# Kernel optimization log

Measured on AMD Instinct MI355X. Metric: run time of the kernel, lower is better.

Reference implementation:

```python
import jax, jax.numpy as jnp
import numpy as np

B, S0, S1 = 4, 768, 256
T = S0 + S1
D0, D1 = 2048, 1024
N, K, H = 8, 1, 256  # num_heads, num_kv_heads, head_dim
G = N // K
BIG_NEG = -2.3819763e38


def _apply_rope(x, positions, max_wavelength=10000):
    # x: [B, L, Hn, Hd]; positions: [B, L] float32
    half = x.shape[-1] // 2
    freq_exponents = (2.0 / x.shape[-1]) * jnp.arange(half, dtype=jnp.float32)
    timescale = max_wavelength ** freq_exponents
    radians = positions[..., None] / timescale[None, None, :]   # [B, L, half]
    radians = radians[..., None, :]                             # [B, L, 1, half]
    sin, cos = jnp.sin(radians), jnp.cos(radians)
    x1, x2 = jnp.split(x, 2, axis=-1)
    res = jnp.concatenate([x1 * cos - x2 * sin, x2 * cos + x1 * sin], axis=-1)
    return res.astype(x.dtype)


def setup_inputs() -> dict:
    key = jax.random.key(0)
    ks = jax.random.split(key, 8)
    x0 = jax.random.normal(ks[0], (B, S0, D0), dtype=jnp.float32)
    x1 = jax.random.normal(ks[1], (B, S1, D1), dtype=jnp.float32)
    positions = jnp.broadcast_to(jnp.arange(T, dtype=jnp.float32), (B, T))
    # causal mask [B, 1, T, T]
    attn_mask = jnp.broadcast_to(jnp.tril(jnp.ones((T, T), dtype=bool)), (B, 1, T, T))
    # lecun_normal-style init: std = 1/sqrt(fan_in=width)
    q0_w = jax.random.normal(ks[2], (N, D0, H), dtype=jnp.float32) * (D0 ** -0.5)
    kv0_w = jax.random.normal(ks[3], (2, K, D0, H), dtype=jnp.float32) * (D0 ** -0.5)
    q1_w = jax.random.normal(ks[4], (N, D1, H), dtype=jnp.float32) * (D1 ** -0.5)
    kv1_w = jax.random.normal(ks[5], (2, K, D1, H), dtype=jnp.float32) * (D1 ** -0.5)
    o0_w = jax.random.normal(ks[6], (N, H, D0), dtype=jnp.float32) * ((N * H) ** -0.5)
    o1_w = jax.random.normal(ks[7], (N, H, D1), dtype=jnp.float32) * ((N * H) ** -0.5)
    return {"x0": x0, "x1": x1, "positions": positions, "attn_mask": attn_mask,
            "q0_w": q0_w, "kv0_w": kv0_w, "q1_w": q1_w, "kv1_w": kv1_w,
            "o0_w": o0_w, "o1_w": o1_w}


def reference(x0, x1, positions, attn_mask, q0_w, kv0_w, q1_w, kv1_w, o0_w, o1_w):
    dtype = x0.dtype
    # per-stream GQA projections (num_kv_heads != num_heads path)
    q_a = jnp.einsum('BTD,NDH->BTNH', x0, q0_w)
    kv_a = jnp.einsum('BSD,CKDH->CBSKH', x0, kv0_w)
    q_b = jnp.einsum('BTD,NDH->BTNH', x1, q1_w)
    kv_b = jnp.einsum('BSD,CKDH->CBSKH', x1, kv1_w)
    # concat streams along sequence
    q = jnp.concatenate([q_a, q_b], axis=1)                 # [B, T, N, H]
    k = jnp.concatenate([kv_a[0], kv_b[0]], axis=1)         # [B, T, K, H]
    v = jnp.concatenate([kv_a[1], kv_b[1]], axis=1)         # [B, T, K, H]
    # inline RoPE + query scaling
    q = _apply_rope(q, positions) * (H ** -0.5)
    k = _apply_rope(k, positions)
    # GQA grouping: N = K * G
    qg = q.reshape(q.shape[0], q.shape[1], K, G, H)          # [B, T, K, G, H]
    logits = jnp.einsum('BTKGH,BSKH->BKGTS', qg, k,
                        preferred_element_type=jnp.float32)  # fp32 scores
    masked = jnp.where(attn_mask[:, :, None, :, :], logits, BIG_NEG)
    probs = jax.nn.softmax(masked, axis=-1).astype(dtype)
    encoded = jnp.einsum('BKGTS,BSKH->BTKGH', probs, v)
    encoded = encoded.reshape(encoded.shape[0], encoded.shape[1], N, H)  # [B, T, N, H]
    out0 = jnp.einsum('BTNH,NHD->BTD', encoded[:, :S0], o0_w)
    out1 = jnp.einsum('BTNH,NHD->BTD', encoded[:, S0:], o1_w)
    return (out0, out1)
```

## Files before the change

kernel.cpp:

```cpp
#include <hip/hip_runtime.h>

typedef unsigned short u16;
typedef __attribute__((ext_vector_type(8))) short bf16x8;
typedef __attribute__((ext_vector_type(4))) float f32x4;

#define CB   4
#define CS0  768
#define CS1  256
#define CT   1024
#define CD0  2048
#define CD1  1024
#define CN   8
#define CH   256
#define IDENT (1 << 30)
#define BIGBASE 0x7fffffff

__device__ __forceinline__ float bf2f(u16 u) {
    union { unsigned int i; float f; } v;
    v.i = ((unsigned int)u) << 16;
    return v.f;
}
__device__ __forceinline__ u16 f2bf(float f) {
    union { float f; unsigned int i; } v;
    v.f = f;
    unsigned int r = 0x7fffu + ((v.i >> 16) & 1u);
    return (u16)((v.i + r) >> 16);
}

__device__ __forceinline__ void gl_lds16(const u16* g, u16* lds_base) {
    __builtin_amdgcn_global_load_lds(
        (const __attribute__((address_space(1))) void*)g,
        (__attribute__((address_space(3))) void*)lds_base,
        16, 0, 0);
}

struct PSeg { const float* in; u16* out; int R, C, base, lgx, lgy, mode; };
struct PSeg8 { PSeg t[8]; };

__global__ __launch_bounds__(256) void prep_multi(PSeg8 segs)
{
    __shared__ float tl[32][33];
    int bid = blockIdx.x;
    PSeg g = segs.t[0];
    #pragma unroll
    for (int i = 1; i < 8; i++)
        if (bid >= segs.t[i].base) g = segs.t[i];
    int r = bid - g.base;
    if (g.mode == 0) {
        int i = r * 256 + threadIdx.x;
        float4 v = ((const float4*)g.in)[i];
        ushort4 o;
        o.x = f2bf(v.x); o.y = f2bf(v.y); o.z = f2bf(v.z); o.w = f2bf(v.w);
        ((ushort4*)g.out)[i] = o;
    } else {
        int bx = r & ((1 << g.lgx) - 1);
        int by = (r >> g.lgx) & ((1 << g.lgy) - 1);
        int bz = r >> (g.lgx + g.lgy);
        const float* in = g.in + (size_t)bz * g.R * g.C;
        u16* out = g.out + (size_t)bz * g.R * g.C;
        int c0 = bx * 32, r0 = by * 32;
        int tx = threadIdx.x & 31, ty = threadIdx.x >> 5;
        #pragma unroll
        for (int i = 0; i < 32; i += 8)
            tl[ty + i][tx] = in[(size_t)(r0 + ty + i) * g.C + c0 + tx];
        __syncthreads();
        #pragma unroll
        for (int i = 0; i < 32; i += 8)
            out[(size_t)(c0 + ty + i) * g.R + r0 + tx] = f2bf(tl[tx][ty + i]);
    }
}

struct GSeg {
    const u16* A; const u16* BT; void* C;
    int K, Cstride, base, lgnx;
    int Sa, Ta, ta, Sc, Tc, tc, obf, pad;
};
struct GSeg4 { GSeg s[4]; };

__global__ __launch_bounds__(512, 2) void gemm256_multi(GSeg4 segs)
{
    extern __shared__ __align__(16) u16 lds[];

    int bid = blockIdx.x;
    GSeg g = segs.s[0];
    if (bid >= segs.s[1].base) g = segs.s[1];
    if (bid >= segs.s[2].base) g = segs.s[2];
    if (bid >= segs.s[3].base) g = segs.s[3];

    int tid  = threadIdx.x;
    int r    = bid - g.base;
    int n0   = (r & ((1 << g.lgnx) - 1)) * 256;
    int m0   = (r >> g.lgnx) * 256;
    int wave = tid >> 6, lane = tid & 63;
    int wr   = wave >> 2, wc = wave & 3;

    int srow  = tid >> 2;
    int skoff = ((tid & 3) ^ ((srow >> 1) & 3)) * 8;
    int am0 = m0 + srow, am1 = m0 + 128 + srow;
    const u16* aptr0 = g.A + (size_t)((am0 / g.Sa) * g.Ta + g.ta + am0 % g.Sa) * g.K + skoff;
    const u16* aptr1 = g.A + (size_t)((am1 / g.Sa) * g.Ta + g.ta + am1 % g.Sa) * g.K + skoff;
    const u16* bptr0 = g.BT + (size_t)(n0 + srow) * g.K + skoff;
    const u16* bptr1 = g.BT + (size_t)(n0 + 128 + srow) * g.K + skoff;

    int l15 = lane & 15, q4 = lane >> 4;
    int swz = (q4 ^ ((l15 >> 1) & 3)) * 8;

#define STAGE_A(tt) do { int kk = (tt) * 32; \
        u16* d = lds + ((tt) & 3) * 16384 + tid * 8; \
        gl_lds16(aptr0 + kk, d); gl_lds16(aptr1 + kk, d + 4096); } while (0)
#define STAGE_B(tt) do { int kk = (tt) * 32; \
        u16* d = lds + ((tt) & 3) * 16384 + 8192 + tid * 8; \
        gl_lds16(bptr0 + kk, d); gl_lds16(bptr1 + kk, d + 4096); } while (0)

    f32x4 acc[8][4] = {};
    int nkt = g.K >> 5;

    STAGE_A(0); STAGE_B(0);
    STAGE_A(1); STAGE_B(1);
    STAGE_A(2); STAGE_B(2);

    for (int t = 0; t < nkt; ++t) {
        if (t + 2 < nkt)      asm volatile("s_waitcnt vmcnt(8)" ::: "memory");
        else if (t + 1 < nkt) asm volatile("s_waitcnt vmcnt(4)" ::: "memory");
        else                  asm volatile("s_waitcnt vmcnt(0)" ::: "memory");
        __builtin_amdgcn_sched_barrier(0);
        __builtin_amdgcn_s_barrier();
        asm volatile("" ::: "memory");

        const u16* At = lds + (t & 3) * 16384;
        const u16* Bt = At + 8192;

        bf16x8 af[8], bf0, bf1;
        #pragma unroll
        for (int m = 0; m < 8; ++m)
            af[m] = *(const bf16x8*)&At[(wr * 128 + m * 16 + l15) * 32 + swz];
        bf0 = *(const bf16x8*)&Bt[(wc * 64 +  0 + l15) * 32 + swz];
        bf1 = *(const bf16x8*)&Bt[(wc * 64 + 16 + l15) * 32 + swz];
        if (t + 3 < nkt) STAGE_A(t + 3);
        __builtin_amdgcn_s_barrier();
        __builtin_amdgcn_s_setprio(1);
        #pragma unroll
        for (int m = 0; m < 8; ++m) {
            acc[m][0] = __builtin_amdgcn_mfma_f32_16x16x32_bf16(af[m], bf0, acc[m][0], 0, 0, 0);
            acc[m][1] = __builtin_amdgcn_mfma_f32_16x16x32_bf16(af[m], bf1, acc[m][1], 0, 0, 0);
        }
        __builtin_amdgcn_s_setprio(0);

        bf16x8 bg0 = *(const bf16x8*)&Bt[(wc * 64 + 32 + l15) * 32 + swz];
        bf16x8 bg1 = *(const bf16x8*)&Bt[(wc * 64 + 48 + l15) * 32 + swz];
        if (t + 3 < nkt) STAGE_B(t + 3);
        __builtin_amdgcn_s_barrier();
        __builtin_amdgcn_s_setprio(1);
        #pragma unroll
        for (int m = 0; m < 8; ++m) {
            acc[m][2] = __builtin_amdgcn_mfma_f32_16x16x32_bf16(af[m], bg0, acc[m][2], 0, 0, 0);
            acc[m][3] = __builtin_amdgcn_mfma_f32_16x16x32_bf16(af[m], bg1, acc[m][3], 0, 0, 0);
        }
        __builtin_amdgcn_s_setprio(0);
    }
#undef STAGE_A
#undef STAGE_B

    #pragma unroll
    for (int m = 0; m < 8; ++m) {
        #pragma unroll
        for (int rr = 0; rr < 4; ++rr) {
            int mm = m0 + wr * 128 + m * 16 + q4 * 4 + rr;
            int grow = (mm / g.Sc) * g.Tc + g.tc + mm % g.Sc;
            if (g.obf) {
                u16* crow = (u16*)g.C + (size_t)grow * g.Cstride + n0 + wc * 64 + l15;
                #pragma unroll
                for (int n = 0; n < 4; ++n)
                    crow[n * 16] = f2bf(acc[m][n][rr]);
            } else {
                float* crow = (float*)g.C + (size_t)grow * g.Cstride + n0 + wc * 64 + l15;
                #pragma unroll
                for (int n = 0; n < 4; ++n)
                    crow[n * 16] = acc[m][n][rr];
            }
        }
    }
}

__global__ __launch_bounds__(256) void rope_vt_kernel(
    const u16* __restrict__ qsrc, const u16* __restrict__ kvsrc,
    const float* __restrict__ positions,
    u16* __restrict__ qb, u16* __restrict__ kb, u16* __restrict__ vto)
{
    int bid = blockIdx.x;
    if (bid < 18432) {
        int idx = bid * 256 + threadIdx.x;
        const int QP = CB * CT * CN * 128;
        if (idx < QP) {
            int h  = idx & 127;
            int n  = (idx >> 7) & 7;
            int bt = idx >> 10;
            const u16* base = qsrc + (size_t)bt * 2048 + n * 256;
            float pos = positions[bt];
            float ts  = powf(10000.0f, (float)h * (1.0f / 128.0f));
            float rr  = pos / ts;
            float sn = sinf(rr), cs = cosf(rr);
            float x1 = bf2f(base[h]), x2 = bf2f(base[h + 128]);
            u16* ob = qb + (size_t)bt * 2048 + n * 256;
            ob[h]       = f2bf((x1 * cs - x2 * sn) * 0.0625f);
            ob[h + 128] = f2bf((x2 * cs + x1 * sn) * 0.0625f);
        } else {
            int j  = idx - QP;
            int h  = j & 127;
            int bt = j >> 7;
            const u16* base = kvsrc + (size_t)bt * 512;
            float pos = positions[bt];
            float ts  = powf(10000.0f, (float)h * (1.0f / 128.0f));
            float rr  = pos / ts;
            float sn = sinf(rr), cs = cosf(rr);
            float x1 = bf2f(base[h]), x2 = bf2f(base[h + 128]);
            int b = bt >> 10, t = bt & 1023;
            int h2 = h + 128;
            kb[((size_t)(b * 8 + (h  >> 5)) * 1024 + t) * 32 + (h  & 31)] = f2bf(x1 * cs - x2 * sn);
            kb[((size_t)(b * 8 + (h2 >> 5)) * 1024 + t) * 32 + (h2 & 31)] = f2bf(x2 * cs + x1 * sn);
        }
    } else {
        int vb = bid - 18432;
        int h  = threadIdx.x;
        int sc = vb & 31;
        int b  = vb >> 5;
        const u16* src = kvsrc + ((size_t)(b * 1024 + sc * 32) * 512 + 256 + h);
        u16* dst = vto + ((size_t)(b * 32 + sc) * 256 + h) * 32;
        u16 buf[32];
        #pragma unroll
        for (int ss = 0; ss < 32; ss++)
            buf[ss] = src[(size_t)ss * 512];
        #pragma unroll
        for (int i = 0; i < 8; i++)
            ((ushort4*)dst)[i] = ((ushort4*)buf)[i];
    }
}

__global__ __launch_bounds__(256) void flash_attn(
    const u16* __restrict__ qb, const u16* __restrict__ kb,
    const u16* __restrict__ vt, u16* __restrict__ encoded)
{
    __shared__ __align__(16) u16 Ks[8 * 64 * 32];
    __shared__ __align__(16) u16 Vs[2 * 256 * 32];
    __shared__ __align__(16) u16 Pw[4][16 * 72];

    int tid  = threadIdx.x;
    int wave = tid >> 6, lane = tid & 63;
    int q4 = lane >> 4, l15 = lane & 15;
    int swz = (q4 ^ ((l15 >> 1) & 3)) * 8;

    int bid  = blockIdx.x;
    int half = bid >> 8;
    int r    = bid & 255;
    int b    = (half << 1) | (r >> 7);
    int ti   = r & 127;
    if (half) ti = 127 - ti;
    int t0 = ti * 8;

    bf16x8 af[8];
    {
        int m = wave * 16 + l15;
        int head = m >> 3, tl = m & 7;
        const u16* qrow = qb + ((size_t)(b * CT + t0 + tl) * 2048 + head * 256 + q4 * 8);
        #pragma unroll
        for (int kc = 0; kc < 8; kc++)
            af[kc] = *(const bf16x8*)(qrow + kc * 32);
    }

    f32x4 O[16] = {};
    float lrun[4] = {0.f, 0.f, 0.f, 0.f};

    int send = t0 + 8;
    for (int s0 = 0; s0 < send; s0 += 64) {
        bool lastTile = (s0 + 64 >= send);
        if (s0) __syncthreads();
        #pragma unroll
        for (int is = 0; is < 8; is++) {
            int ubase = is * 256 + wave * 64;
            int u = ubase + lane;
            int s = (u >> 2) & 63, hc = u >> 8;
            int ug = (u & 3) ^ ((s >> 1) & 3);
            const u16* g = kb + ((size_t)((b * 8 + hc) * 1024 + s0 + s) * 32 + ug * 8);
            gl_lds16(g, Ks + (size_t)ubase * 8);
        }
        #pragma unroll
        for (int is = 0; is < 8; is++) {
            int ubase = is * 256 + wave * 64;
            int u = ubase + lane;
            int h = (u >> 2) & 255;
            int vg = (u & 3) ^ ((h >> 1) & 3);
            const u16* g = vt + ((size_t)(b * 32 + (s0 >> 5)) * 8192 + (size_t)(u >> 2) * 32 + vg * 8);
            gl_lds16(g, Vs + (size_t)ubase * 8);
        }
        __syncthreads();

        f32x4 P[4];
        #pragma unroll
        for (int ni = 0; ni < 4; ni++) {
            f32x4 c = {};
            #pragma unroll
            for (int kc = 0; kc < 8; kc++) {
                bf16x8 bfr = *(const bf16x8*)&Ks[kc * 2048 + (ni * 16 + l15) * 32 + swz];
                c = __builtin_amdgcn_mfma_f32_16x16x32_bf16(af[kc], bfr, c, 0, 0, 0);
            }
            P[ni] = c;
        }

        if (lastTile) {
            #pragma unroll
            for (int ni = 0; ni < 4; ni++)
                #pragma unroll
                for (int rr = 0; rr < 4; rr++) {
                    int trow = t0 + ((q4 * 4 + rr) & 7);
                    int scol = s0 + ni * 16 + l15;
                    if (scol > trow) P[ni][rr] = -3.0e38f;
                }
        }

        #pragma unroll
        for (int ni = 0; ni < 4; ni++)
            #pragma unroll
            for (int rr = 0; rr < 4; rr++) {
                float e = __expf(P[ni][rr]);
                P[ni][rr] = e;
                Pw[wave][(q4 * 4 + rr) * 72 + ni * 16 + l15] = f2bf(e);
            }
        #pragma unroll
        for (int rr = 0; rr < 4; rr++) {
            float s = (P[0][rr] + P[1][rr]) + (P[2][rr] + P[3][rr]);
            s += __shfl_xor(s, 1);
            s += __shfl_xor(s, 2);
            s += __shfl_xor(s, 4);
            s += __shfl_xor(s, 8);
            lrun[rr] += s;
        }

        bf16x8 pa0 = *(const bf16x8*)&Pw[wave][l15 * 72 + q4 * 8];
        bf16x8 pa1 = *(const bf16x8*)&Pw[wave][l15 * 72 + 32 + q4 * 8];
        #pragma unroll
        for (int nc = 0; nc < 16; nc++) {
            bf16x8 b0 = *(const bf16x8*)&Vs[(nc * 16 + l15) * 32 + swz];
            bf16x8 b1 = *(const bf16x8*)&Vs[8192 + (nc * 16 + l15) * 32 + swz];
            O[nc] = __builtin_amdgcn_mfma_f32_16x16x32_bf16(pa0, b0, O[nc], 0, 0, 0);
            O[nc] = __builtin_amdgcn_mfma_f32_16x16x32_bf16(pa1, b1, O[nc], 0, 0, 0);
        }
    }

    #pragma unroll
    for (int rr = 0; rr < 4; rr++) {
        int mm = wave * 16 + q4 * 4 + rr;
        int hd = mm >> 3, tl = mm & 7;
        u16* erow = encoded + ((size_t)(b * CT + t0 + tl) * 2048 + hd * 256 + l15);
        float inv = 1.0f / lrun[rr];
        #pragma unroll
        for (int nc = 0; nc < 16; nc++)
            erow[nc * 16] = f2bf(O[nc][rr] * inv);
    }
}

extern "C" void kernel_launch(void* const* d_in, const int* in_sizes, int n_in,
                              void* d_out, int out_size, void* d_ws, size_t ws_size,
                              hipStream_t stream)
{
    const float* x0        = (const float*)d_in[0];
    const float* x1        = (const float*)d_in[1];
    const float* positions = (const float*)d_in[2];
    const float* q0_w  = (const float*)d_in[4];
    const float* kv0_w = (const float*)d_in[5];
    const float* q1_w  = (const float*)d_in[6];
    const float* kv1_w = (const float*)d_in[7];
    const float* o0_w  = (const float*)d_in[8];
    const float* o1_w  = (const float*)d_in[9];
    float* out = (float*)d_out;

    static int attr_done = 0;
    if (!attr_done) {
        hipFuncSetAttribute((const void*)gemm256_multi,
                            hipFuncAttributeMaxDynamicSharedMemorySize, 131072);
        attr_done = 1;
    }

    char* W = (char*)d_ws;
    u16* qbuf16  = (u16*)(W);
    u16* kvbuf16 = (u16*)(W + 16777216);
    u16* WTo0  = (u16*)(W + 20971520);
    u16* WTo1  = (u16*)(W + 29360128);
    u16* x0b   = (u16*)(W + 33554432);
    u16* x1b   = (u16*)(W + 46137344);
    u16* WTq0  = (u16*)(W + 48234496);
    u16* WTkv0 = (u16*)(W + 56623104);
    u16* WTq1  = (u16*)(W + 58720256);
    u16* WTkv1 = (u16*)(W + 62914560);
    u16* qb  = x0b;
    u16* kb  = WTkv0;
    u16* vtb = WTq1;
    u16* encoded = qbuf16;

    PSeg8 ps8;
    ps8.t[0] = { x0,    x0b,      0,    0,     0, 0, 0, 0 };
    ps8.t[1] = { x1,    x1b,      0,    0,  6144, 0, 0, 0 };
    ps8.t[2] = { q0_w,  WTq0,  2048,  256,  7168, 3, 6, 1 };
    ps8.t[3] = { kv0_w, WTkv0, 2048,  256, 11264, 3, 6, 1 };
    ps8.t[4] = { q1_w,  WTq1,  1024,  256, 12288, 3, 5, 1 };
    ps8.t[5] = { kv1_w, WTkv1, 1024,  256, 14336, 3, 5, 1 };
    ps8.t[6] = { o0_w,  WTo0,  2048, 2048, 14848, 6, 6, 1 };
    ps8.t[7] = { o1_w,  WTo1,  2048, 1024, 18944, 5, 6, 1 };
    prep_multi<<<dim3(20992), dim3(256), 0, stream>>>(ps8);

    GSeg4 ps;
    ps.s[0] = { x0b, WTq0,  qbuf16,  2048, 2048,   0, 3, IDENT, 0, 0, CS0, CT, 0,   1, 0 };
    ps.s[1] = { x0b, WTkv0, kvbuf16, 2048,  512,  96, 1, IDENT, 0, 0, CS0, CT, 0,   1, 0 };
    ps.s[2] = { x1b, WTq1,  qbuf16,  1024, 2048, 120, 3, IDENT, 0, 0, CS1, CT, CS0, 1, 0 };
    ps.s[3] = { x1b, WTkv1, kvbuf16, 1024,  512, 152, 1, IDENT, 0, 0, CS1, CT, CS0, 1, 0 };
    gemm256_multi<<<dim3(160), dim3(512), 131072, stream>>>(ps);

    rope_vt_kernel<<<dim3(18560), dim3(256), 0, stream>>>(
        qbuf16, kvbuf16, positions, qb, kb, vtb);

    flash_attn<<<dim3(512), dim3(256), 0, stream>>>(qb, kb, vtb, encoded);

    GSeg4 os;
    os.s[0] = { encoded, WTo0, out, 2048, 2048, 0, 3, CS0, CT, 0, IDENT, 0, 0, 0, 0 };
    os.s[1] = { encoded, WTo1, out + (size_t)CB * CS0 * CD0,
                2048, 1024, 96, 2, CS1, CT, CS0, IDENT, 0, 0, 0, 0 };
    os.s[2] = { nullptr, nullptr, nullptr, 32, 0, BIGBASE, 0, 1, 0, 0, 1, 0, 0, 0, 0 };
    os.s[3] = { nullptr, nullptr, nullptr, 32, 0, BIGBASE, 0, 1, 0, 0, 1, 0, 0, 0, 0 };
    gemm256_multi<<<dim3(112), dim3(512), 131072, stream>>>(os);
}
```

Measured before the change: 328.7 us.

## Remap GEMM tiles across XCDs and split MFMA loop into 4x4 register sub-blocks

```diff
diff --git a/kernel.cpp b/kernel.cpp
--- a/kernel.cpp
+++ b/kernel.cpp
@@ -73,7 +73,7 @@
 struct GSeg {
     const u16* A; const u16* BT; void* C;
     int K, Cstride, base, lgnx;
-    int Sa, Ta, ta, Sc, Tc, tc, obf, pad;
+    int Sa, Ta, ta, Sc, Tc, tc, obf, cpx;
 };
 struct GSeg4 { GSeg s[4]; };
 
@@ -89,6 +89,7 @@
 
     int tid  = threadIdx.x;
     int r    = bid - g.base;
+    r = (r & 7) * g.cpx + (r >> 3);
     int n0   = (r & ((1 << g.lgnx) - 1)) * 256;
     int m0   = (r >> g.lgnx) * 256;
     int wave = tid >> 6, lane = tid & 63;
@@ -130,32 +131,42 @@
         const u16* At = lds + (t & 3) * 16384;
         const u16* Bt = At + 8192;
 
-        bf16x8 af[8], bf0, bf1;
-        #pragma unroll
-        for (int m = 0; m < 8; ++m)
-            af[m] = *(const bf16x8*)&At[(wr * 128 + m * 16 + l15) * 32 + swz];
-        bf0 = *(const bf16x8*)&Bt[(wc * 64 +  0 + l15) * 32 + swz];
-        bf1 = *(const bf16x8*)&Bt[(wc * 64 + 16 + l15) * 32 + swz];
+        bf16x8 af0[4], bfr[4];
+        #pragma unroll
+        for (int m = 0; m < 4; ++m)
+            af0[m] = *(const bf16x8*)&At[(wr * 128 + m * 16 + l15) * 32 + swz];
+        #pragma unroll
+        for (int n = 0; n < 4; ++n)
+            bfr[n] = *(const bf16x8*)&Bt[(wc * 64 + n * 16 + l15) * 32 + swz];
         if (t + 3 < nkt) STAGE_A(t + 3);
         __builtin_amdgcn_s_barrier();
+        asm volatile("s_waitcnt lgkmcnt(0)" ::: "memory");
+        __builtin_amdgcn_sched_barrier(0);
         __builtin_amdgcn_s_setprio(1);
         #pragma unroll
-        for (int m = 0; m < 8; ++m) {
-            acc[m][0] = __builtin_amdgcn_mfma_f32_16x16x32_bf16(af[m], bf0, acc[m][0], 0, 0, 0);
-            acc[m][1] = __builtin_amdgcn_mfma_f32_16x16x32_bf16(af[m], bf1, acc[m][1], 0, 0, 0);
-        }
+        for (int m = 0; m < 4; ++m)
+            #pragma unroll
+            for (int n = 0; n < 4; ++n)
+                acc[m][n] = __builtin_amdgcn_mfma_f32_16x16x32_bf16(
+                    af0[m], bfr[n], acc[m][n], 0, 0, 0);
         __builtin_amdgcn_s_setprio(0);
-
-        bf16x8 bg0 = *(const bf16x8*)&Bt[(wc * 64 + 32 + l15) * 32 + swz];
-        bf16x8 bg1 = *(const bf16x8*)&Bt[(wc * 64 + 48 + l15) * 32 + swz];
+        __builtin_amdgcn_s_barrier();
+
+        bf16x8 af1[4];
+        #pragma unroll
+        for (int m = 0; m < 4; ++m)
+            af1[m] = *(const bf16x8*)&At[(wr * 128 + (m + 4) * 16 + l15) * 32 + swz];
         if (t + 3 < nkt) STAGE_B(t + 3);
         __builtin_amdgcn_s_barrier();
+        asm volatile("s_waitcnt lgkmcnt(0)" ::: "memory");
+        __builtin_amdgcn_sched_barrier(0);
         __builtin_amdgcn_s_setprio(1);
         #pragma unroll
-        for (int m = 0; m < 8; ++m) {
-            acc[m][2] = __builtin_amdgcn_mfma_f32_16x16x32_bf16(af[m], bg0, acc[m][2], 0, 0, 0);
-            acc[m][3] = __builtin_amdgcn_mfma_f32_16x16x32_bf16(af[m], bg1, acc[m][3], 0, 0, 0);
-        }
+        for (int m = 0; m < 4; ++m)
+            #pragma unroll
+            for (int n = 0; n < 4; ++n)
+                acc[m + 4][n] = __builtin_amdgcn_mfma_f32_16x16x32_bf16(
+                    af1[m], bfr[n], acc[m + 4][n], 0, 0, 0);
         __builtin_amdgcn_s_setprio(0);
     }
 #undef STAGE_A
@@ -408,10 +419,10 @@
     prep_multi<<<dim3(20992), dim3(256), 0, stream>>>(ps8);
 
     GSeg4 ps;
-    ps.s[0] = { x0b, WTq0,  qbuf16,  2048, 2048,   0, 3, IDENT, 0, 0, CS0, CT, 0,   1, 0 };
-    ps.s[1] = { x0b, WTkv0, kvbuf16, 2048,  512,  96, 1, IDENT, 0, 0, CS0, CT, 0,   1, 0 };
-    ps.s[2] = { x1b, WTq1,  qbuf16,  1024, 2048, 120, 3, IDENT, 0, 0, CS1, CT, CS0, 1, 0 };
-    ps.s[3] = { x1b, WTkv1, kvbuf16, 1024,  512, 152, 1, IDENT, 0, 0, CS1, CT, CS0, 1, 0 };
+    ps.s[0] = { x0b, WTq0,  qbuf16,  2048, 2048,   0, 3, IDENT, 0, 0, CS0, CT, 0,   1, 12 };
+    ps.s[1] = { x0b, WTkv0, kvbuf16, 2048,  512,  96, 1, IDENT, 0, 0, CS0, CT, 0,   1,  3 };
+    ps.s[2] = { x1b, WTq1,  qbuf16,  1024, 2048, 120, 3, IDENT, 0, 0, CS1, CT, CS0, 1,  4 };
+    ps.s[3] = { x1b, WTkv1, kvbuf16, 1024,  512, 152, 1, IDENT, 0, 0, CS1, CT, CS0, 1,  1 };
     gemm256_multi<<<dim3(160), dim3(512), 131072, stream>>>(ps);
 
     rope_vt_kernel<<<dim3(18560), dim3(256), 0, stream>>>(
@@ -420,10 +431,10 @@
     flash_attn<<<dim3(512), dim3(256), 0, stream>>>(qb, kb, vtb, encoded);
 
     GSeg4 os;
-    os.s[0] = { encoded, WTo0, out, 2048, 2048, 0, 3, CS0, CT, 0, IDENT, 0, 0, 0, 0 };
+    os.s[0] = { encoded, WTo0, out, 2048, 2048, 0, 3, CS0, CT, 0, IDENT, 0, 0, 0, 12 };
     os.s[1] = { encoded, WTo1, out + (size_t)CB * CS0 * CD0,
-                2048, 1024, 96, 2, CS1, CT, CS0, IDENT, 0, 0, 0, 0 };
-    os.s[2] = { nullptr, nullptr, nullptr, 32, 0, BIGBASE, 0, 1, 0, 0, 1, 0, 0, 0, 0 };
-    os.s[3] = { nullptr, nullptr, nullptr, 32, 0, BIGBASE, 0, 1, 0, 0, 1, 0, 0, 0, 0 };
+                2048, 1024, 96, 2, CS1, CT, CS0, IDENT, 0, 0, 0, 2 };
+    os.s[2] = { nullptr, nullptr, nullptr, 32, 0, BIGBASE, 0, 1, 0, 0, 1, 0, 0, 1 };
+    os.s[3] = { nullptr, nullptr, nullptr, 32, 0, BIGBASE, 0, 1, 0, 0, 1, 0, 0, 1 };
     gemm256_multi<<<dim3(112), dim3(512), 131072, stream>>>(os);
 }
```

New measurement: 335.4 us. 2.0% more time.
